# Kernel tuning notes

Hardware: AMD Instinct MI355X
Metric: run time of the kernel (lower is better)

## Reference

```python
import jax, jax.numpy as jnp
import numpy as np

N_NODES = 1_000_000
MAX_DEG = 64
BATCH = 16384
NUM_SAMPLES = 32


def setup_inputs() -> dict:
    key = jax.random.key(0)
    k1, k2, k3, k4, k5 = jax.random.split(key, 5)
    adj_info = jax.random.randint(k1, (N_NODES, MAX_DEG), 0, N_NODES, dtype=jnp.int32)
    # temporal adjacency lists are time-sorted; mask-count = valid prefix length
    ts_info = jnp.sort(jax.random.uniform(k2, (N_NODES, MAX_DEG), dtype=jnp.float32), axis=1)
    ids = jax.random.randint(k3, (BATCH,), 0, N_NODES, dtype=jnp.int32)
    tss = jax.random.uniform(k4, (BATCH,), dtype=jnp.float32)
    # pre-drawn uniforms replace the per-row tf.random.uniform calls (deterministic)
    u = jax.random.uniform(k5, (BATCH, NUM_SAMPLES), dtype=jnp.float32)
    return {"ids": ids, "tss": tss, "adj_info": adj_info, "ts_info": ts_info,
            "u": u, "batch_size": BATCH, "num_samples": NUM_SAMPLES}


def reference(ids, tss, adj_info, ts_info, u, batch_size, num_samples):
    adj_lists = jnp.take(adj_info, ids, axis=0)          # [B, D]
    ts_lists = jnp.take(ts_info, ids, axis=0)            # [B, D]
    mask = ts_lists < tss[:, None]                       # edges strictly before current ts
    counts = jnp.sum(mask.astype(jnp.int32), axis=1)     # [B] valid-prefix length
    err = jnp.maximum(counts, 1)                         # avoid 0 bound
    # bounded sampling: col_i ~ Uniform{0..err_i-1}
    col = jnp.minimum((u * err[:, None].astype(u.dtype)).astype(jnp.int32),
                      err[:, None] - 1)                  # [B, S]
    rows = jnp.arange(batch_size, dtype=jnp.int32)[:, None]
    valid = (counts > 0)[:, None]                        # rows with no valid edge -> zeroed
    neighbors = (valid.astype(adj_lists.dtype) * adj_lists[rows, col]).reshape(-1)  # [B*S]
    ts_out = (valid.astype(ts_lists.dtype) * ts_lists[rows, col]).reshape(-1)       # [B*S]
    return neighbors, ts_out
```

## Files before the change

### kernel.cpp

```cpp
#include <hip/hip_runtime.h>


#define MAX_DEG 64

__global__ __launch_bounds__(256) void MaskNeighborSampler_kernel(
    const int* __restrict__ ids,
    const float* __restrict__ tss,
    const int* __restrict__ adj,
    const float* __restrict__ tsi,
    const float* __restrict__ u,
    float* __restrict__ out_nbr,
    float* __restrict__ out_ts,
    int B, int S) {
  const int gtid = blockIdx.x * blockDim.x + threadIdx.x;
  const int row  = gtid >> 6;
  const int lane = threadIdx.x & 63;
  if (row >= B) return;

  const int   id = ids[row];
  const float t  = tss[row];
  const long long base = (long long)id * MAX_DEG;

  const int   adjv = adj[base + lane];
  const float tsv  = tsi[base + lane];

  const unsigned long long m = __ballot(tsv < t);
  const int count = __popcll(m);
  const int err   = count > 0 ? count : 1;
  const float errf = (float)err;

  const int   sidx = lane & (S - 1);
  const float uu   = u[(long long)row * S + sidx];
  int col = (int)(uu * errf);
  const int cmax = err - 1;
  if (col > cmax) col = cmax;

  const int   nb = __shfl(adjv, col, 64);
  const float tv = __shfl(tsv,  col, 64);

  if (lane < S) {
    const long long o = (long long)row * S + lane;
    const bool valid = count > 0;
    out_nbr[o] = valid ? (float)nb : 0.0f;
    out_ts[o]  = valid ? tv        : 0.0f;
  }
}

extern "C" void kernel_launch(void* const* d_in, const int* in_sizes, int n_in,
                              void* d_out, int out_size, void* d_ws, size_t ws_size,
                              hipStream_t stream) {
  const int*   ids = (const int*)  d_in[0];
  const float* tss = (const float*)d_in[1];
  const int*   adj = (const int*)  d_in[2];
  const float* tsi = (const float*)d_in[3];
  const float* u   = (const float*)d_in[4];
  const int B = in_sizes[0];
  const int S = in_sizes[4] / B;

  float* out_nbr = (float*)d_out;
  float* out_ts  = out_nbr + (long long)B * S;

  const int threads = 256;
  const int rows_per_block = threads / 64;
  const int grid = (B + rows_per_block - 1) / rows_per_block;
  MaskNeighborSampler_kernel<<<grid, threads, 0, stream>>>(
      ids, tss, adj, tsi, u, out_nbr, out_ts, B, S);
}
```

Measured before the change: 9.721 us.

## Process two rows per wavefront so all 64 lanes store output

Each 64-lane wavefront now handles two batch rows: it loads both adjacency rows, computes both counts with two ballots, and lanes 0-31 sample for row A while lanes 32-63 sample for row B. Every lane loads a u value and writes output, so the half-idle lanes of the old layout are gone and the grid is halved. More gathers are in flight per wave to hide random-access latency. The sample count is hardcoded to 32, and an odd B would write past the last row.

```diff
diff --git a/kernel.cpp b/kernel.cpp
--- a/kernel.cpp
+++ b/kernel.cpp
@@ -2,6 +2,7 @@
 
 
 #define MAX_DEG 64
+#define NSAMP   32
 
 __global__ __launch_bounds__(256) void MaskNeighborSampler_kernel(
     const int* __restrict__ ids,
@@ -11,39 +12,46 @@
     const float* __restrict__ u,
     float* __restrict__ out_nbr,
     float* __restrict__ out_ts,
-    int B, int S) {
-  const int gtid = blockIdx.x * blockDim.x + threadIdx.x;
-  const int row  = gtid >> 6;
+    int B) {
+  const int wave = (blockIdx.x * blockDim.x + threadIdx.x) >> 6;
   const int lane = threadIdx.x & 63;
-  if (row >= B) return;
+  const int rowA = wave * 2;
+  if (rowA >= B) return;
+  const int rowB = (rowA + 1 < B) ? rowA + 1 : rowA;
 
-  const int   id = ids[row];
-  const float t  = tss[row];
-  const long long base = (long long)id * MAX_DEG;
+  const int   idA = ids[rowA];
+  const int   idB = ids[rowB];
+  const float tA  = tss[rowA];
+  const float tB  = tss[rowB];
 
-  const int   adjv = adj[base + lane];
-  const float tsv  = tsi[base + lane];
+  const int offA = idA * MAX_DEG + lane;
+  const int offB = idB * MAX_DEG + lane;
+  const int   adjA = adj[offA];
+  const int   adjB = adj[offB];
+  const float tsA  = tsi[offA];
+  const float tsB  = tsi[offB];
 
-  const unsigned long long m = __ballot(tsv < t);
-  const int count = __popcll(m);
-  const int err   = count > 0 ? count : 1;
-  const float errf = (float)err;
+  const size_t obase = (size_t)rowA * NSAMP;
+  const float uu = u[obase + lane];
 
-  const int   sidx = lane & (S - 1);
-  const float uu   = u[(long long)row * S + sidx];
-  int col = (int)(uu * errf);
-  const int cmax = err - 1;
-  if (col > cmax) col = cmax;
+  const int cntA = __popcll(__ballot(tsA < tA));
+  const int cntB = __popcll(__ballot(tsB < tB));
+  const int errA = cntA > 0 ? cntA : 1;
+  const int errB = cntB > 0 ? cntB : 1;
 
-  const int   nb = __shfl(adjv, col, 64);
-  const float tv = __shfl(tsv,  col, 64);
+  const bool lo  = lane < NSAMP;
+  const int  err = lo ? errA : errB;
+  int col = (int)(uu * (float)err);
+  if (col > err - 1) col = err - 1;
 
-  if (lane < S) {
-    const long long o = (long long)row * S + lane;
-    const bool valid = count > 0;
-    out_nbr[o] = valid ? (float)nb : 0.0f;
-    out_ts[o]  = valid ? tv        : 0.0f;
-  }
+  const int   nA = __shfl(adjA, col, 64);
+  const int   nB = __shfl(adjB, col, 64);
+  const float vA = __shfl(tsA,  col, 64);
+  const float vB = __shfl(tsB,  col, 64);
+
+  const bool valid = lo ? (cntA > 0) : (cntB > 0);
+  out_nbr[obase + lane] = valid ? (float)(lo ? nA : nB) : 0.0f;
+  out_ts [obase + lane] = valid ? (lo ? vA : vB)        : 0.0f;
 }
 
 extern "C" void kernel_launch(void* const* d_in, const int* in_sizes, int n_in,
@@ -55,14 +63,13 @@
   const float* tsi = (const float*)d_in[3];
   const float* u   = (const float*)d_in[4];
   const int B = in_sizes[0];
-  const int S = in_sizes[4] / B;
 
   float* out_nbr = (float*)d_out;
-  float* out_ts  = out_nbr + (long long)B * S;
+  float* out_ts  = out_nbr + (size_t)B * NSAMP;
 
+  const int waves = (B + 1) / 2;
   const int threads = 256;
-  const int rows_per_block = threads / 64;
-  const int grid = (B + rows_per_block - 1) / rows_per_block;
+  const int grid = (waves * 64 + threads - 1) / threads;
   MaskNeighborSampler_kernel<<<grid, threads, 0, stream>>>(
-      ids, tss, adj, tsi, u, out_nbr, out_ts, B, S);
+      ids, tss, adj, tsi, u, out_nbr, out_ts, B);
 }
```

After: 10.04 us. 3.3% more time.

## Pack four rows per wave with vectorized int4/float4 loads and float2 outputs

Applied to the files above, without the earlier changes.

Each wave now handles four rows, with 16 lanes per row loading the adjacency and timestamp rows as int4/float4. The valid-edge count comes from a 16-lane xor-shuffle reduction instead of a full-wave ballot. Each lane samples two columns and gathers them with shuffles plus a 4-way select, then writes float2 outputs, so the idle half-wave stores of the old version go away. This cuts the wave count by four and widens memory transactions, at the cost of many more shuffles per lane. It also hardcodes 32 samples per row.

```diff
diff --git a/kernel.cpp b/kernel.cpp
--- a/kernel.cpp
+++ b/kernel.cpp
@@ -1,49 +1,75 @@
 #include <hip/hip_runtime.h>
 
 
-#define MAX_DEG 64
+#define NSAMP 32
+
+__device__ __forceinline__ float sel4(float x, float y, float z, float w, int e) {
+  float lo = (e & 1) ? y : x;
+  float hi = (e & 1) ? w : z;
+  return (e & 2) ? hi : lo;
+}
 
 __global__ __launch_bounds__(256) void MaskNeighborSampler_kernel(
     const int* __restrict__ ids,
     const float* __restrict__ tss,
-    const int* __restrict__ adj,
-    const float* __restrict__ tsi,
-    const float* __restrict__ u,
-    float* __restrict__ out_nbr,
-    float* __restrict__ out_ts,
-    int B, int S) {
-  const int gtid = blockIdx.x * blockDim.x + threadIdx.x;
-  const int row  = gtid >> 6;
+    const int4* __restrict__ adj4,
+    const float4* __restrict__ tsi4,
+    const float2* __restrict__ u2,
+    float2* __restrict__ out_nbr2,
+    float2* __restrict__ out_ts2,
+    int B) {
+  const int wave = (blockIdx.x * blockDim.x + threadIdx.x) >> 6;
   const int lane = threadIdx.x & 63;
-  if (row >= B) return;
+  const int g    = lane >> 4;
+  const int k16  = lane & 15;
+  int row = wave * 4 + g;
+  if (wave * 4 >= B) return;
+  if (row >= B) row = B - 1;
 
   const int   id = ids[row];
   const float t  = tss[row];
-  const long long base = (long long)id * MAX_DEG;
 
-  const int   adjv = adj[base + lane];
-  const float tsv  = tsi[base + lane];
+  const float4 ts4 = tsi4[(size_t)id * 16 + k16];
+  const int4   ad4 = adj4[(size_t)id * 16 + k16];
 
-  const unsigned long long m = __ballot(tsv < t);
-  const int count = __popcll(m);
+  int cnt = (int)(ts4.x < t) + (int)(ts4.y < t) + (int)(ts4.z < t) + (int)(ts4.w < t);
+  cnt += __shfl_xor(cnt, 1, 16);
+  cnt += __shfl_xor(cnt, 2, 16);
+  cnt += __shfl_xor(cnt, 4, 16);
+  cnt += __shfl_xor(cnt, 8, 16);
+  const int count = cnt;
   const int err   = count > 0 ? count : 1;
   const float errf = (float)err;
 
-  const int   sidx = lane & (S - 1);
-  const float uu   = u[(long long)row * S + sidx];
-  int col = (int)(uu * errf);
-  const int cmax = err - 1;
-  if (col > cmax) col = cmax;
+  const float a0 = (float)ad4.x, a1 = (float)ad4.y, a2 = (float)ad4.z, a3 = (float)ad4.w;
 
-  const int   nb = __shfl(adjv, col, 64);
-  const float tv = __shfl(tsv,  col, 64);
+  const float2 uu = u2[(size_t)wave * 64 + lane];
+  const int gbase = lane & 48;
+  const int cmax  = err - 1;
 
-  if (lane < S) {
-    const long long o = (long long)row * S + lane;
-    const bool valid = count > 0;
-    out_nbr[o] = valid ? (float)nb : 0.0f;
-    out_ts[o]  = valid ? tv        : 0.0f;
-  }
+  int c0 = (int)(uu.x * errf); if (c0 > cmax) c0 = cmax;
+  int c1 = (int)(uu.y * errf); if (c1 > cmax) c1 = cmax;
+  const int s0 = gbase + (c0 >> 2), e0 = c0 & 3;
+  const int s1 = gbase + (c1 >> 2), e1 = c1 & 3;
+
+  const float t0x = __shfl(ts4.x, s0, 64), t0y = __shfl(ts4.y, s0, 64);
+  const float t0z = __shfl(ts4.z, s0, 64), t0w = __shfl(ts4.w, s0, 64);
+  const float n0x = __shfl(a0, s0, 64),    n0y = __shfl(a1, s0, 64);
+  const float n0z = __shfl(a2, s0, 64),    n0w = __shfl(a3, s0, 64);
+  const float t1x = __shfl(ts4.x, s1, 64), t1y = __shfl(ts4.y, s1, 64);
+  const float t1z = __shfl(ts4.z, s1, 64), t1w = __shfl(ts4.w, s1, 64);
+  const float n1x = __shfl(a0, s1, 64),    n1y = __shfl(a1, s1, 64);
+  const float n1z = __shfl(a2, s1, 64),    n1w = __shfl(a3, s1, 64);
+
+  const bool valid = count > 0;
+  float2 onbr, ots;
+  onbr.x = valid ? sel4(n0x, n0y, n0z, n0w, e0) : 0.0f;
+  onbr.y = valid ? sel4(n1x, n1y, n1z, n1w, e1) : 0.0f;
+  ots.x  = valid ? sel4(t0x, t0y, t0z, t0w, e0) : 0.0f;
+  ots.y  = valid ? sel4(t1x, t1y, t1z, t1w, e1) : 0.0f;
+
+  out_nbr2[(size_t)wave * 64 + lane] = onbr;
+  out_ts2 [(size_t)wave * 64 + lane] = ots;
 }
 
 extern "C" void kernel_launch(void* const* d_in, const int* in_sizes, int n_in,
@@ -55,14 +81,14 @@
   const float* tsi = (const float*)d_in[3];
   const float* u   = (const float*)d_in[4];
   const int B = in_sizes[0];
-  const int S = in_sizes[4] / B;
 
   float* out_nbr = (float*)d_out;
-  float* out_ts  = out_nbr + (long long)B * S;
+  float* out_ts  = out_nbr + (size_t)B * NSAMP;
 
+  const int waves   = (B + 3) / 4;
   const int threads = 256;
-  const int rows_per_block = threads / 64;
-  const int grid = (B + rows_per_block - 1) / rows_per_block;
+  const int grid    = (waves * 64 + threads - 1) / threads;
   MaskNeighborSampler_kernel<<<grid, threads, 0, stream>>>(
-      ids, tss, adj, tsi, u, out_nbr, out_ts, B, S);
+      ids, tss, (const int4*)adj, (const float4*)tsi, (const float2*)u,
+      (float2*)out_nbr, (float2*)out_ts, B);
 }
```

Measured after the change: 10.28 us. 5.8% more time.
